# Performance work log

Hardware: AMD Instinct MI355X
Metric: run time of the kernel (lower is better)

The kernel has to match this reference:

```python
import jax, jax.numpy as jnp
import numpy as np

T, IN, INTER, OUT = 4096, 1024, 1024, 1024

def setup_inputs() -> dict:
    key = jax.random.key(0)
    ks = jax.random.split(key, 11)
    s_in = 1.0 / np.sqrt(IN)
    s_int = 1.0 / np.sqrt(INTER)
    return {
        "x": jax.random.normal(ks[0], (T, IN), dtype=jnp.float32),
        "d_gamma": jax.random.uniform(ks[1], (T, T), dtype=jnp.float32),
        "Wq": jax.random.uniform(ks[2], (IN, INTER), jnp.float32, -s_in, s_in),
        "bq": jax.random.uniform(ks[3], (INTER,), jnp.float32, -s_in, s_in),
        "Wk": jax.random.uniform(ks[4], (IN, INTER), jnp.float32, -s_in, s_in),
        "bk": jax.random.uniform(ks[5], (INTER,), jnp.float32, -s_in, s_in),
        "Wv": jax.random.uniform(ks[6], (IN, INTER), jnp.float32, -s_in, s_in),
        "bv": jax.random.uniform(ks[7], (INTER,), jnp.float32, -s_in, s_in),
        "Wr": jax.random.uniform(ks[8], (INTER, OUT), jnp.float32, -s_int, s_int),
        "br": jax.random.uniform(ks[9], (OUT,), jnp.float32, -s_int, s_int),
        "prelu_a": jnp.asarray(0.25, dtype=jnp.float32),
    }

def reference(x, d_gamma, Wq, bq, Wk, bk, Wv, bv, Wr, br, prelu_a):
    num_node = x.shape[0]
    xr = x.reshape(T, IN)
    q = xr @ Wq + bq                      # [T, INTER]
    k = xr @ Wk + bk                      # [T, INTER]
    v = xr @ Wv + bv                      # [T, INTER]
    scores = q @ k.T                      # [T, T] retention scores
    retained = (d_gamma * scores) @ v     # decay-masked aggregation, [T, INTER]
    out = retained @ Wr + br              # [T, OUT]
    out = jnp.where(out >= 0, out, prelu_a * out)  # PReLU
    return out.reshape(num_node, -1)
```

## Files before the change

kernel.cpp:

```cpp
#include <hip/hip_runtime.h>

#define TT 4096
#define DIN 1024

typedef _Float16 f16;
typedef __attribute__((ext_vector_type(8))) _Float16 f16x8;
typedef __attribute__((ext_vector_type(4))) float f32x4;

__device__ f16 g_xh[TT * DIN];
__device__ f16 g_wqkvT[3 * DIN * DIN];
__device__ f16 g_wrT[DIN * DIN];
__device__ f16 g_q[TT * DIN];
__device__ f16 g_k[TT * DIN];
__device__ f16 g_v[TT * DIN];
__device__ f16 g_vT[DIN * TT];
__device__ f16 g_sg[(size_t)TT * TT];
__device__ f16 g_part[4][TT * DIN];
__device__ f16 g_ret[TT * DIN];

__global__ void prep_cast_x(const float* __restrict__ x) {
    int i = blockIdx.x * 256 + threadIdx.x;
    g_xh[i] = (f16)x[i];
}

__global__ void prep_transpose(const float* __restrict__ Wq, const float* __restrict__ Wk,
                               const float* __restrict__ Wv, const float* __restrict__ Wr) {
    int idx = blockIdx.x * 256 + threadIdx.x;
    int which = blockIdx.y;
    const float* src = (which == 0) ? Wq : (which == 1) ? Wk : (which == 2) ? Wv : Wr;
    f16* dst = (which < 3) ? (g_wqkvT + (size_t)which * DIN * DIN) : g_wrT;
    int j = idx >> 10, k = idx & 1023;
    dst[idx] = (f16)src[k * DIN + j];
}

__global__ __launch_bounds__(256) void transpose_v() {
    __shared__ f16 t[64][72];
    const int bc = blockIdx.x;
    const int br = blockIdx.y;
    const int tdx = threadIdx.x;
    const int r0 = tdx >> 3;
    const int c8 = (tdx & 7) * 8;
#pragma unroll
    for (int p = 0; p < 2; ++p) {
        int r = r0 + p * 32;
        *(f16x8*)&t[r][c8] = *(const f16x8*)&g_v[(size_t)(br * 64 + r) * DIN + bc * 64 + c8];
    }
    __syncthreads();
#pragma unroll
    for (int p = 0; p < 2; ++p) {
        int c = r0 + p * 32;
        f16x8 v;
#pragma unroll
        for (int j = 0; j < 8; ++j) v[j] = t[c8 + j][c];
        *(f16x8*)&g_vT[(size_t)(bc * 64 + c) * TT + br * 64 + c8] = v;
    }
}

__device__ __forceinline__ void gload_lds16(const void* g, void* l) {
    __builtin_amdgcn_global_load_lds(
        (const __attribute__((address_space(1))) unsigned int*)g,
        (__attribute__((address_space(3))) unsigned int*)l,
        16, 0, 0);
}

template <int EPI>
__global__ __launch_bounds__(512, 2) void gemm8(const float* __restrict__ gamma,
                                                const float* __restrict__ bq,
                                                const float* __restrict__ bk,
                                                const float* __restrict__ bv,
                                                const float* __restrict__ br,
                                                const float* __restrict__ prelu_a,
                                                float* __restrict__ out) {
    constexpr int NT  = 16;
    constexpr int ld2A = (EPI == 2) ? 8192 : 2048;
    constexpr int ld2B = (EPI == 2) ? 8192 : 2048;

    const f16* Ap = (EPI == 0) ? g_xh : (EPI == 1) ? g_q : (EPI == 2) ? g_sg : g_ret;
    const f16* Bp = (EPI == 0) ? g_wqkvT : (EPI == 1) ? g_k : (EPI == 2) ? g_vT : g_wrT;
    const int kb_base = (EPI == 2) ? blockIdx.z * 2048 : 0;

    __shared__ __align__(16) char smem[131072];

    const int t = threadIdx.x;
    const int w = t >> 6, l = t & 63;
    const int wr = w >> 2, wc = w & 3;
    const int fr = l & 15;
    const int fkb = (l >> 4) * 16;
    const int arow0 = blockIdx.y * 256;
    const int bcol0 = blockIdx.x * 256;

    auto stage = [&](const f16* M, int ld2, int row0, int kb0, int dstoff) {
#pragma unroll
        for (int r = 0; r < 2; ++r) {
            int off = r * 8192 + w * 1024;
            int row = (off + l * 16) >> 7;
            int cb  = (l & 7) * 16;
            int scb = cb ^ ((row & 7) << 4);
            const char* src = (const char*)M + (size_t)(row0 + row) * ld2 + kb0 + scb;
            gload_lds16(src, smem + dstoff + off);
        }
    };

    auto ldsA = [&](int c, int m, int ks) -> f16x8 {
        int lr = m * 16 + fr;
        int kb = ks * 64 + fkb;
        return *(const f16x8*)(smem + c * 65536 + wr * 16384 + lr * 128 + (kb ^ ((lr & 7) << 4)));
    };
    auto ldsB = [&](int c, int n, int ks) -> f16x8 {
        int lc = (wc & 1) * 64 + n * 16 + fr;
        int kb = ks * 64 + fkb;
        return *(const f16x8*)(smem + c * 65536 + 32768 + (wc >> 1) * 16384 + lc * 128 + (kb ^ ((lc & 7) << 4)));
    };

#define KB(kt) (kb_base + (kt) * 128)

    stage(Ap, ld2A, arow0,       KB(0), 0);
    stage(Ap, ld2A, arow0 + 128, KB(0), 16384);
    stage(Bp, ld2B, bcol0,       KB(0), 32768);
    stage(Bp, ld2B, bcol0 + 128, KB(0), 49152);
    stage(Bp, ld2B, bcol0,       KB(1), 65536 + 32768);
    stage(Bp, ld2B, bcol0 + 128, KB(1), 65536 + 49152);

    f32x4 acc[8][4] = {};
    f16x8 bf[4][2];

#define GPHASE(MB, STAGE_STMT)                                              \
    {                                                                       \
        f16x8 af[2][2];                                                     \
        _Pragma("unroll") for (int i = 0; i < 2; ++i)                       \
            _Pragma("unroll") for (int ks = 0; ks < 2; ++ks)                \
                af[i][ks] = ldsA(c, (MB) + i, ks);                          \
        STAGE_STMT;                                                         \
        __builtin_amdgcn_s_barrier();                                       \
        __builtin_amdgcn_s_setprio(1);                                      \
        _Pragma("unroll") for (int i = 0; i < 2; ++i)                       \
            _Pragma("unroll") for (int n = 0; n < 4; ++n)                   \
                _Pragma("unroll") for (int ks = 0; ks < 2; ++ks)            \
                    acc[(MB) + i][n] = __builtin_amdgcn_mfma_f32_16x16x32_f16( \
                        af[i][ks], bf[n][ks], acc[(MB) + i][n], 0, 0, 0);   \
        __builtin_amdgcn_s_setprio(0);                                      \
        __builtin_amdgcn_s_barrier();                                       \
    }

    for (int kt = 0; kt < NT; ++kt) {
        const int c = kt & 1;
        if (kt == NT - 1) asm volatile("s_waitcnt vmcnt(0)" ::: "memory");
        else              asm volatile("s_waitcnt vmcnt(4)" ::: "memory");
        __builtin_amdgcn_s_barrier();
#pragma unroll
        for (int n = 0; n < 4; ++n)
#pragma unroll
            for (int ks = 0; ks < 2; ++ks) bf[n][ks] = ldsB(c, n, ks);
        GPHASE(0, if (kt + 1 < NT) stage(Ap, ld2A, arow0,       KB(kt + 1), (c ^ 1) * 65536))
        GPHASE(2, if (kt + 1 < NT) stage(Ap, ld2A, arow0 + 128, KB(kt + 1), (c ^ 1) * 65536 + 16384))
        GPHASE(4, if (kt + 2 < NT) stage(Bp, ld2B, bcol0,       KB(kt + 2), c * 65536 + 32768))
        GPHASE(6, if (kt + 2 < NT) stage(Bp, ld2B, bcol0 + 128, KB(kt + 2), c * 65536 + 49152))
    }
#undef GPHASE
#undef KB

    const int rb = (l >> 4) * 4;
    const int crow0 = arow0 + wr * 128;
    const int ccol0 = bcol0 + wc * 64;

    if constexpr (EPI == 0) {
        const int sel = blockIdx.x >> 2;
        f16* dst = (sel == 0) ? g_q : (sel == 1) ? g_k : g_v;
        const float* bias = (sel == 0) ? bq : (sel == 1) ? bk : bv;
        const int cb0 = ccol0 - sel * 1024;
#pragma unroll
        for (int m = 0; m < 8; ++m)
#pragma unroll
            for (int n = 0; n < 4; ++n) {
                const int cl = cb0 + n * 16 + fr;
                const float bsum = bias[cl];
#pragma unroll
                for (int j = 0; j < 4; ++j)
                    dst[(size_t)(crow0 + m * 16 + rb + j) * 1024 + cl] = (f16)(acc[m][n][j] + bsum);
            }
    } else if constexpr (EPI == 1) {
        __syncthreads();
        const float* gl = (const float*)smem;
#pragma unroll 1
        for (int h = 0; h < 2; ++h) {
#pragma unroll
            for (int rr = 0; rr < 16; ++rr) {
                const char* src = (const char*)(gamma + (size_t)(arow0 + h * 128 + rr * 8 + w) * TT + bcol0) + l * 16;
                gload_lds16(src, smem + rr * 8192 + w * 1024);
            }
            __syncthreads();
            if (wr == h) {
#pragma unroll
                for (int m = 0; m < 8; ++m)
#pragma unroll
                    for (int n = 0; n < 4; ++n) {
                        const int lcol = wc * 64 + n * 16 + fr;
#pragma unroll
                        for (int j = 0; j < 4; ++j) {
                            const int lrow = m * 16 + rb + j;
                            const float g = gl[lrow * 256 + lcol];
                            g_sg[(size_t)(crow0 + lrow) * TT + bcol0 + lcol] = (f16)(acc[m][n][j] * g);
                        }
                    }
            }
            __syncthreads();
        }
    } else if constexpr (EPI == 2) {
        f16* gp = g_part[blockIdx.z];
#pragma unroll
        for (int m = 0; m < 8; ++m)
#pragma unroll
            for (int n = 0; n < 4; ++n) {
                const int cl = ccol0 + n * 16 + fr;
#pragma unroll
                for (int j = 0; j < 4; ++j)
                    gp[(size_t)(crow0 + m * 16 + rb + j) * 1024 + cl] = (f16)acc[m][n][j];
            }
    } else {
        const float pa = *prelu_a;
#pragma unroll
        for (int m = 0; m < 8; ++m)
#pragma unroll
            for (int n = 0; n < 4; ++n) {
                const int cl = ccol0 + n * 16 + fr;
                const float bsum = br[cl];
#pragma unroll
                for (int j = 0; j < 4; ++j) {
                    float o = acc[m][n][j] + bsum;
                    o = (o >= 0.f) ? o : pa * o;
                    out[(size_t)(crow0 + m * 16 + rb + j) * 1024 + cl] = o;
                }
            }
    }
}

__global__ __launch_bounds__(256) void reduce_parts() {
    size_t i = (size_t)(blockIdx.x * 256 + threadIdx.x) * 8;
    f16x8 a = *(const f16x8*)&g_part[0][i];
    f16x8 b = *(const f16x8*)&g_part[1][i];
    f16x8 cc = *(const f16x8*)&g_part[2][i];
    f16x8 d = *(const f16x8*)&g_part[3][i];
    f16x8 o;
#pragma unroll
    for (int j = 0; j < 8; ++j)
        o[j] = (f16)((float)a[j] + (float)b[j] + (float)cc[j] + (float)d[j]);
    *(f16x8*)&g_ret[i] = o;
}

extern "C" void kernel_launch(void* const* d_in, const int* in_sizes, int n_in,
                              void* d_out, int out_size, void* d_ws, size_t ws_size,
                              hipStream_t stream) {
    const float* x     = (const float*)d_in[0];
    const float* gamma = (const float*)d_in[1];
    const float* Wq    = (const float*)d_in[2];
    const float* bq    = (const float*)d_in[3];
    const float* Wk    = (const float*)d_in[4];
    const float* bk    = (const float*)d_in[5];
    const float* Wv    = (const float*)d_in[6];
    const float* bv    = (const float*)d_in[7];
    const float* Wr    = (const float*)d_in[8];
    const float* br    = (const float*)d_in[9];
    const float* pa    = (const float*)d_in[10];
    float* out = (float*)d_out;

    prep_cast_x<<<TT * DIN / 256, 256, 0, stream>>>(x);
    prep_transpose<<<dim3(DIN * DIN / 256, 4), 256, 0, stream>>>(Wq, Wk, Wv, Wr);

    gemm8<0><<<dim3(12, 16), 512, 0, stream>>>(gamma, bq, bk, bv, br, pa, out);
    transpose_v<<<dim3(16, 64), 256, 0, stream>>>();
    gemm8<1><<<dim3(16, 16), 512, 0, stream>>>(gamma, bq, bk, bv, br, pa, out);
    gemm8<2><<<dim3(4, 16, 4), 512, 0, stream>>>(gamma, bq, bk, bv, br, pa, out);
    reduce_parts<<<TT * DIN / 8 / 256, 256, 0, stream>>>();
    gemm8<3><<<dim3(4, 16), 512, 0, stream>>>(gamma, bq, bk, bv, br, pa, out);
}
```

Before: 200.6 us.

## Stage GEMM epilogues through LDS for coalesced stores, split-K final GEMM

Every GEMM epilogue now writes its accumulators to swizzled LDS and then reads them back row-contiguously. This allows vectorized, coalesced stores and coalesced vector loads of gamma, replacing per-element strided stores and the async gamma load into LDS. The final output GEMM is split 4-way along K to fill more CUs, with a new reduce_out kernel that sums the fp16 partials and applies bias and PReLU. The x cast is vectorized 8-wide. The split adds an extra pass over the partials and rounds them to fp16 before the final sum.

```diff
diff --git a/kernel.cpp b/kernel.cpp
--- a/kernel.cpp
+++ b/kernel.cpp
@@ -5,6 +5,7 @@
 
 typedef _Float16 f16;
 typedef __attribute__((ext_vector_type(8))) _Float16 f16x8;
+typedef __attribute__((ext_vector_type(4))) _Float16 f16x4;
 typedef __attribute__((ext_vector_type(4))) float f32x4;
 
 __device__ f16 g_xh[TT * DIN];
@@ -18,9 +19,14 @@
 __device__ f16 g_part[4][TT * DIN];
 __device__ f16 g_ret[TT * DIN];
 
-__global__ void prep_cast_x(const float* __restrict__ x) {
-    int i = blockIdx.x * 256 + threadIdx.x;
-    g_xh[i] = (f16)x[i];
+__global__ __launch_bounds__(256) void prep_cast_x(const float* __restrict__ x) {
+    int i = (blockIdx.x * 256 + threadIdx.x) * 8;
+    f32x4 a = *(const f32x4*)&x[i];
+    f32x4 b = *(const f32x4*)&x[i + 4];
+    f16x8 o;
+#pragma unroll
+    for (int j = 0; j < 4; ++j) { o[j] = (f16)a[j]; o[j + 4] = (f16)b[j]; }
+    *(f16x8*)&g_xh[i] = o;
 }
 
 __global__ void prep_transpose(const float* __restrict__ Wq, const float* __restrict__ Wk,
@@ -71,13 +77,14 @@
                                                 const float* __restrict__ br,
                                                 const float* __restrict__ prelu_a,
                                                 float* __restrict__ out) {
-    constexpr int NT  = 16;
+    constexpr int NT  = (EPI == 3) ? 4 : 16;
     constexpr int ld2A = (EPI == 2) ? 8192 : 2048;
     constexpr int ld2B = (EPI == 2) ? 8192 : 2048;
 
     const f16* Ap = (EPI == 0) ? g_xh : (EPI == 1) ? g_q : (EPI == 2) ? g_sg : g_ret;
     const f16* Bp = (EPI == 0) ? g_wqkvT : (EPI == 1) ? g_k : (EPI == 2) ? g_vT : g_wrT;
-    const int kb_base = (EPI == 2) ? blockIdx.z * 2048 : 0;
+    const int kb_base = (EPI == 2) ? blockIdx.z * 2048
+                      : (EPI == 3) ? blockIdx.z * 512 : 0;
 
     __shared__ __align__(16) char smem[131072];
 
@@ -160,77 +167,63 @@
 #undef KB
 
     const int rb = (l >> 4) * 4;
-    const int crow0 = arow0 + wr * 128;
-    const int ccol0 = bcol0 + wc * 64;
-
+
+    const int sel0 = (EPI == 0) ? (int)(blockIdx.x >> 2) : 0;
+    f16* dst0 = nullptr;
+    const float* bias0 = nullptr;
     if constexpr (EPI == 0) {
-        const int sel = blockIdx.x >> 2;
-        f16* dst = (sel == 0) ? g_q : (sel == 1) ? g_k : g_v;
-        const float* bias = (sel == 0) ? bq : (sel == 1) ? bk : bv;
-        const int cb0 = ccol0 - sel * 1024;
-#pragma unroll
-        for (int m = 0; m < 8; ++m)
-#pragma unroll
-            for (int n = 0; n < 4; ++n) {
-                const int cl = cb0 + n * 16 + fr;
-                const float bsum = bias[cl];
-#pragma unroll
-                for (int j = 0; j < 4; ++j)
-                    dst[(size_t)(crow0 + m * 16 + rb + j) * 1024 + cl] = (f16)(acc[m][n][j] + bsum);
+        dst0 = (sel0 == 0) ? g_q : (sel0 == 1) ? g_k : g_v;
+        bias0 = (sel0 == 0) ? bq : (sel0 == 1) ? bk : bv;
+    }
+    f16* gp = nullptr;
+    if constexpr (EPI == 2 || EPI == 3) gp = g_part[blockIdx.z];
+
+    __syncthreads();
+#pragma unroll 1
+    for (int h = 0; h < 2; ++h) {
+        if (wr == h) {
+#pragma unroll
+            for (int m = 0; m < 8; ++m)
+#pragma unroll
+                for (int n = 0; n < 4; ++n)
+#pragma unroll
+                    for (int j = 0; j < 4; ++j) {
+                        const int lr = m * 16 + rb + j;
+                        const int cb = (wc * 64 + n * 16 + fr) * 4;
+                        *(float*)(smem + lr * 1024 + (cb ^ ((lr & 7) << 4))) = acc[m][n][j];
+                    }
+        }
+        __syncthreads();
+#pragma unroll
+        for (int it = 0; it < 16; ++it) {
+            const int f  = t + it * 512;
+            const int lr = f >> 6;
+            const int cb = (f & 63) * 16;
+            const f32x4 vv = *(const f32x4*)(smem + lr * 1024 + (cb ^ ((lr & 7) << 4)));
+            const int row = arow0 + h * 128 + lr;
+            const int c4  = cb >> 2;
+            if constexpr (EPI == 0) {
+                const int colg = bcol0 - sel0 * 1024 + c4;
+                const f32x4 b4 = *(const f32x4*)&bias0[colg];
+                f16x4 o;
+#pragma unroll
+                for (int j = 0; j < 4; ++j) o[j] = (f16)(vv[j] + b4[j]);
+                *(f16x4*)&dst0[(size_t)row * 1024 + colg] = o;
+            } else if constexpr (EPI == 1) {
+                const size_t gi = (size_t)row * TT + bcol0 + c4;
+                const f32x4 g4 = *(const f32x4*)&gamma[gi];
+                f16x4 o;
+#pragma unroll
+                for (int j = 0; j < 4; ++j) o[j] = (f16)(vv[j] * g4[j]);
+                *(f16x4*)&g_sg[gi] = o;
+            } else {
+                f16x4 o;
+#pragma unroll
+                for (int j = 0; j < 4; ++j) o[j] = (f16)vv[j];
+                *(f16x4*)&gp[(size_t)row * 1024 + bcol0 + c4] = o;
             }
-    } else if constexpr (EPI == 1) {
+        }
         __syncthreads();
-        const float* gl = (const float*)smem;
-#pragma unroll 1
-        for (int h = 0; h < 2; ++h) {
-#pragma unroll
-            for (int rr = 0; rr < 16; ++rr) {
-                const char* src = (const char*)(gamma + (size_t)(arow0 + h * 128 + rr * 8 + w) * TT + bcol0) + l * 16;
-                gload_lds16(src, smem + rr * 8192 + w * 1024);
-            }
-            __syncthreads();
-            if (wr == h) {
-#pragma unroll
-                for (int m = 0; m < 8; ++m)
-#pragma unroll
-                    for (int n = 0; n < 4; ++n) {
-                        const int lcol = wc * 64 + n * 16 + fr;
-#pragma unroll
-                        for (int j = 0; j < 4; ++j) {
-                            const int lrow = m * 16 + rb + j;
-                            const float g = gl[lrow * 256 + lcol];
-                            g_sg[(size_t)(crow0 + lrow) * TT + bcol0 + lcol] = (f16)(acc[m][n][j] * g);
-                        }
-                    }
-            }
-            __syncthreads();
-        }
-    } else if constexpr (EPI == 2) {
-        f16* gp = g_part[blockIdx.z];
-#pragma unroll
-        for (int m = 0; m < 8; ++m)
-#pragma unroll
-            for (int n = 0; n < 4; ++n) {
-                const int cl = ccol0 + n * 16 + fr;
-#pragma unroll
-                for (int j = 0; j < 4; ++j)
-                    gp[(size_t)(crow0 + m * 16 + rb + j) * 1024 + cl] = (f16)acc[m][n][j];
-            }
-    } else {
-        const float pa = *prelu_a;
-#pragma unroll
-        for (int m = 0; m < 8; ++m)
-#pragma unroll
-            for (int n = 0; n < 4; ++n) {
-                const int cl = ccol0 + n * 16 + fr;
-                const float bsum = br[cl];
-#pragma unroll
-                for (int j = 0; j < 4; ++j) {
-                    float o = acc[m][n][j] + bsum;
-                    o = (o >= 0.f) ? o : pa * o;
-                    out[(size_t)(crow0 + m * 16 + rb + j) * 1024 + cl] = o;
-                }
-            }
     }
 }
 
@@ -245,6 +238,33 @@
     for (int j = 0; j < 8; ++j)
         o[j] = (f16)((float)a[j] + (float)b[j] + (float)cc[j] + (float)d[j]);
     *(f16x8*)&g_ret[i] = o;
+}
+
+__global__ __launch_bounds__(256) void reduce_out(const float* __restrict__ br,
+                                                  const float* __restrict__ prelu_a,
+                                                  float* __restrict__ out) {
+    size_t i = (size_t)(blockIdx.x * 256 + threadIdx.x) * 8;
+    f16x8 a = *(const f16x8*)&g_part[0][i];
+    f16x8 b = *(const f16x8*)&g_part[1][i];
+    f16x8 cc = *(const f16x8*)&g_part[2][i];
+    f16x8 d = *(const f16x8*)&g_part[3][i];
+    const float pa = *prelu_a;
+    const int col = (int)(i & 1023);
+    const f32x4 b0 = *(const f32x4*)&br[col];
+    const f32x4 b1 = *(const f32x4*)&br[col + 4];
+    f32x4 o0, o1;
+#pragma unroll
+    for (int j = 0; j < 4; ++j) {
+        float s = (float)a[j] + (float)b[j] + (float)cc[j] + (float)d[j] + b0[j];
+        o0[j] = (s >= 0.f) ? s : pa * s;
+    }
+#pragma unroll
+    for (int j = 0; j < 4; ++j) {
+        float s = (float)a[j + 4] + (float)b[j + 4] + (float)cc[j + 4] + (float)d[j + 4] + b1[j];
+        o1[j] = (s >= 0.f) ? s : pa * s;
+    }
+    *(f32x4*)&out[i] = o0;
+    *(f32x4*)&out[i + 4] = o1;
 }
 
 extern "C" void kernel_launch(void* const* d_in, const int* in_sizes, int n_in,
@@ -263,7 +283,7 @@
     const float* pa    = (const float*)d_in[10];
     float* out = (float*)d_out;
 
-    prep_cast_x<<<TT * DIN / 256, 256, 0, stream>>>(x);
+    prep_cast_x<<<TT * DIN / 8 / 256, 256, 0, stream>>>(x);
     prep_transpose<<<dim3(DIN * DIN / 256, 4), 256, 0, stream>>>(Wq, Wk, Wv, Wr);
 
     gemm8<0><<<dim3(12, 16), 512, 0, stream>>>(gamma, bq, bk, bv, br, pa, out);
@@ -271,5 +291,6 @@
     gemm8<1><<<dim3(16, 16), 512, 0, stream>>>(gamma, bq, bk, bv, br, pa, out);
     gemm8<2><<<dim3(4, 16, 4), 512, 0, stream>>>(gamma, bq, bk, bv, br, pa, out);
     reduce_parts<<<TT * DIN / 8 / 256, 256, 0, stream>>>();
-    gemm8<3><<<dim3(4, 16), 512, 0, stream>>>(gamma, bq, bk, bv, br, pa, out);
-}
+    gemm8<3><<<dim3(4, 16, 4), 512, 0, stream>>>(gamma, bq, bk, bv, br, pa, out);
+    reduce_out<<<TT * DIN / 8 / 256, 256, 0, stream>>>(br, pa, out);
+}
```

New measurement: 234.5 us. +16.9%, slower.

## Split-K final GEMM with fused reduce epilogue, vectorize cast, swizzle gamma LDS

Applied to the files above, without the earlier changes.

The final Wr GEMM now uses a 4-way split-K grid (64→256 blocks) writing fp16 partials, and a new reduce_out kernel sums them and applies bias and PReLU with vectorized stores. The x cast kernel now processes 8 elements per thread with vector loads and stores. The gamma tile staged into LDS in the scores epilogue is XOR-swizzled to cut bank conflicts, with an explicit vmcnt wait added. The split-K path adds fp16 partial traffic and an extra launch in exchange for better CU occupancy on the small GEMM.

```diff
diff --git a/kernel.cpp b/kernel.cpp
--- a/kernel.cpp
+++ b/kernel.cpp
@@ -5,6 +5,7 @@
 
 typedef _Float16 f16;
 typedef __attribute__((ext_vector_type(8))) _Float16 f16x8;
+typedef __attribute__((ext_vector_type(4))) _Float16 f16x4;
 typedef __attribute__((ext_vector_type(4))) float f32x4;
 
 __device__ f16 g_xh[TT * DIN];
@@ -18,9 +19,14 @@
 __device__ f16 g_part[4][TT * DIN];
 __device__ f16 g_ret[TT * DIN];
 
-__global__ void prep_cast_x(const float* __restrict__ x) {
-    int i = blockIdx.x * 256 + threadIdx.x;
-    g_xh[i] = (f16)x[i];
+__global__ __launch_bounds__(256) void prep_cast_x(const float* __restrict__ x) {
+    int i = (blockIdx.x * 256 + threadIdx.x) * 8;
+    f32x4 a = *(const f32x4*)&x[i];
+    f32x4 b = *(const f32x4*)&x[i + 4];
+    f16x8 o;
+#pragma unroll
+    for (int j = 0; j < 4; ++j) { o[j] = (f16)a[j]; o[j + 4] = (f16)b[j]; }
+    *(f16x8*)&g_xh[i] = o;
 }
 
 __global__ void prep_transpose(const float* __restrict__ Wq, const float* __restrict__ Wk,
@@ -71,13 +77,14 @@
                                                 const float* __restrict__ br,
                                                 const float* __restrict__ prelu_a,
                                                 float* __restrict__ out) {
-    constexpr int NT  = 16;
+    constexpr int NT  = (EPI == 3) ? 4 : 16;
     constexpr int ld2A = (EPI == 2) ? 8192 : 2048;
     constexpr int ld2B = (EPI == 2) ? 8192 : 2048;
 
     const f16* Ap = (EPI == 0) ? g_xh : (EPI == 1) ? g_q : (EPI == 2) ? g_sg : g_ret;
     const f16* Bp = (EPI == 0) ? g_wqkvT : (EPI == 1) ? g_k : (EPI == 2) ? g_vT : g_wrT;
-    const int kb_base = (EPI == 2) ? blockIdx.z * 2048 : 0;
+    const int kb_base = (EPI == 2) ? blockIdx.z * 2048
+                      : (EPI == 3) ? blockIdx.z * 512 : 0;
 
     __shared__ __align__(16) char smem[131072];
 
@@ -180,14 +187,16 @@
             }
     } else if constexpr (EPI == 1) {
         __syncthreads();
-        const float* gl = (const float*)smem;
 #pragma unroll 1
         for (int h = 0; h < 2; ++h) {
 #pragma unroll
             for (int rr = 0; rr < 16; ++rr) {
-                const char* src = (const char*)(gamma + (size_t)(arow0 + h * 128 + rr * 8 + w) * TT + bcol0) + l * 16;
-                gload_lds16(src, smem + rr * 8192 + w * 1024);
-            }
+                const int row = rr * 8 + w;
+                const int cbyte = (l * 16) ^ ((row & 7) << 4);
+                const char* src = (const char*)(gamma + (size_t)(arow0 + h * 128 + row) * TT + bcol0) + cbyte;
+                gload_lds16(src, smem + row * 1024);
+            }
+            asm volatile("s_waitcnt vmcnt(0)" ::: "memory");
             __syncthreads();
             if (wr == h) {
 #pragma unroll
@@ -198,14 +207,14 @@
 #pragma unroll
                         for (int j = 0; j < 4; ++j) {
                             const int lrow = m * 16 + rb + j;
-                            const float g = gl[lrow * 256 + lcol];
-                            g_sg[(size_t)(crow0 + lrow) * TT + bcol0 + lcol] = (f16)(acc[m][n][j] * g);
+                            const float g = *(const float*)(smem + lrow * 1024 + ((lcol * 4) ^ ((lrow & 7) << 4)));
+                            g_sg[(size_t)(arow0 + h * 128 + lrow) * TT + bcol0 + lcol] = (f16)(acc[m][n][j] * g);
                         }
                     }
             }
             __syncthreads();
         }
-    } else if constexpr (EPI == 2) {
+    } else {
         f16* gp = g_part[blockIdx.z];
 #pragma unroll
         for (int m = 0; m < 8; ++m)
@@ -215,21 +224,6 @@
 #pragma unroll
                 for (int j = 0; j < 4; ++j)
                     gp[(size_t)(crow0 + m * 16 + rb + j) * 1024 + cl] = (f16)acc[m][n][j];
-            }
-    } else {
-        const float pa = *prelu_a;
-#pragma unroll
-        for (int m = 0; m < 8; ++m)
-#pragma unroll
-            for (int n = 0; n < 4; ++n) {
-                const int cl = ccol0 + n * 16 + fr;
-                const float bsum = br[cl];
-#pragma unroll
-                for (int j = 0; j < 4; ++j) {
-                    float o = acc[m][n][j] + bsum;
-                    o = (o >= 0.f) ? o : pa * o;
-                    out[(size_t)(crow0 + m * 16 + rb + j) * 1024 + cl] = o;
-                }
             }
     }
 }
@@ -245,6 +239,33 @@
     for (int j = 0; j < 8; ++j)
         o[j] = (f16)((float)a[j] + (float)b[j] + (float)cc[j] + (float)d[j]);
     *(f16x8*)&g_ret[i] = o;
+}
+
+__global__ __launch_bounds__(256) void reduce_out(const float* __restrict__ br,
+                                                  const float* __restrict__ prelu_a,
+                                                  float* __restrict__ out) {
+    size_t i = (size_t)(blockIdx.x * 256 + threadIdx.x) * 8;
+    f16x8 a = *(const f16x8*)&g_part[0][i];
+    f16x8 b = *(const f16x8*)&g_part[1][i];
+    f16x8 cc = *(const f16x8*)&g_part[2][i];
+    f16x8 d = *(const f16x8*)&g_part[3][i];
+    const float pa = *prelu_a;
+    const int col = (int)(i & 1023);
+    const f32x4 b0 = *(const f32x4*)&br[col];
+    const f32x4 b1 = *(const f32x4*)&br[col + 4];
+    f32x4 o0, o1;
+#pragma unroll
+    for (int j = 0; j < 4; ++j) {
+        float s = (float)a[j] + (float)b[j] + (float)cc[j] + (float)d[j] + b0[j];
+        o0[j] = (s >= 0.f) ? s : pa * s;
+    }
+#pragma unroll
+    for (int j = 0; j < 4; ++j) {
+        float s = (float)a[j + 4] + (float)b[j + 4] + (float)cc[j + 4] + (float)d[j + 4] + b1[j];
+        o1[j] = (s >= 0.f) ? s : pa * s;
+    }
+    *(f32x4*)&out[i] = o0;
+    *(f32x4*)&out[i + 4] = o1;
 }
 
 extern "C" void kernel_launch(void* const* d_in, const int* in_sizes, int n_in,
@@ -263,7 +284,7 @@
     const float* pa    = (const float*)d_in[10];
     float* out = (float*)d_out;
 
-    prep_cast_x<<<TT * DIN / 256, 256, 0, stream>>>(x);
+    prep_cast_x<<<TT * DIN / 8 / 256, 256, 0, stream>>>(x);
     prep_transpose<<<dim3(DIN * DIN / 256, 4), 256, 0, stream>>>(Wq, Wk, Wv, Wr);
 
     gemm8<0><<<dim3(12, 16), 512, 0, stream>>>(gamma, bq, bk, bv, br, pa, out);
@@ -271,5 +292,6 @@
     gemm8<1><<<dim3(16, 16), 512, 0, stream>>>(gamma, bq, bk, bv, br, pa, out);
     gemm8<2><<<dim3(4, 16, 4), 512, 0, stream>>>(gamma, bq, bk, bv, br, pa, out);
     reduce_parts<<<TT * DIN / 8 / 256, 256, 0, stream>>>();
-    gemm8<3><<<dim3(4, 16), 512, 0, stream>>>(gamma, bq, bk, bv, br, pa, out);
-}
+    gemm8<3><<<dim3(4, 16, 4), 512, 0, stream>>>(gamma, bq, bk, bv, br, pa, out);
+    reduce_out<<<TT * DIN / 8 / 256, 256, 0, stream>>>(br, pa, out);
+}
```

New measurement: 231.1 us. 1.15x slower.
